# Kernel optimization log

Measured on AMD Instinct MI355X. Metric: run time of the kernel, lower is better.

## Reference

```python
import jax, jax.numpy as jnp
import numpy as np

SIM_THRESHOLD = 0.7
EPS = 1e-8  # matches torch F.cosine_similarity eps

Q, M, D, C = 4096, 65536, 384, 128


def setup_inputs() -> dict:
    key = jax.random.key(0)
    k1, k2, k3 = jax.random.split(key, 3)
    query_embeddings = jax.random.normal(k1, (Q, D), dtype=jnp.float32)
    memory_embeddings = jax.random.normal(k2, (M, D), dtype=jnp.float32)
    # per-example one-hot-ish label vectors [M, C]
    memory_labels = jax.random.uniform(k3, (M, C), dtype=jnp.float32)
    return {
        "query_embeddings": query_embeddings,
        "memory_embeddings": memory_embeddings,
        "memory_labels": memory_labels,
    }


def _l2_normalize(x):
    n = jnp.sqrt(jnp.sum(x * x, axis=-1, keepdims=True))
    return x / jnp.maximum(n, EPS)


def reference(query_embeddings, memory_embeddings, memory_labels):
    # cosine similarity matrix [Q, M] via normalized GEMM
    qn = _l2_normalize(query_embeddings)          # [Q, D]
    mn = _l2_normalize(memory_embeddings)         # [M, D]
    sims = jnp.einsum("qd,md->qm", qn, mn)        # [Q, M]
    max_sim = jnp.max(sims, axis=1)               # [Q]
    max_idx = jnp.argmax(sims, axis=1)            # [Q]
    picked = memory_labels[max_idx]               # [Q, C] gather
    C_ = memory_labels.shape[1]
    uniform = jnp.full((1, C_), 1.0 / C_, dtype=picked.dtype)
    predictions = jnp.where((max_sim > SIM_THRESHOLD)[:, None], picked, uniform)
    return predictions
```

## Files before the change

### kernel.cpp

```cpp
#include <hip/hip_runtime.h>
#include <math.h>

#define QN 4096
#define MN 65536
#define DN 384
#define CN 128
#define NCHUNK 32
#define MROWS_PER_CHUNK (MN / NCHUNK)
#define MT_PER (MROWS_PER_CHUNK / 128)

typedef __attribute__((ext_vector_type(8))) int i32x8;
typedef __attribute__((ext_vector_type(4))) int i32x4;
typedef __attribute__((ext_vector_type(4))) float f32x4;

__device__ __forceinline__ unsigned char f2fp8(float f) {
  return (unsigned char)(__builtin_amdgcn_cvt_pk_fp8_f32(f, 0.f, 0, false) & 0xff);
}

__device__ __forceinline__ void async16(const void* g, void* l) {
  __builtin_amdgcn_global_load_lds(
      (const __attribute__((address_space(1))) unsigned int*)g,
      (__attribute__((address_space(3))) unsigned int*)l, 16, 0, 0);
}

__global__ __launch_bounds__(256) void nrm_kernel(const float* __restrict__ qe,
                                                  const float* __restrict__ me,
                                                  unsigned char* __restrict__ yq,
                                                  unsigned char* __restrict__ ym) {
  const int row = blockIdx.x * 4 + (threadIdx.x >> 6);
  const int lane = threadIdx.x & 63;
  const float* xr;
  unsigned char* yr;
  if (row < QN) {
    xr = qe + (size_t)row * DN;
    yr = yq + (size_t)row * DN;
  } else {
    xr = me + (size_t)(row - QN) * DN;
    yr = ym + (size_t)(row - QN) * DN;
  }
  float v[6];
  float ss = 0.f;
#pragma unroll
  for (int i = 0; i < 6; ++i) {
    v[i] = xr[lane + i * 64];
    ss += v[i] * v[i];
  }
#pragma unroll
  for (int m = 1; m < 64; m <<= 1) ss += __shfl_xor(ss, m);
  const float scale = 1.0f / fmaxf(sqrtf(ss), 1e-8f);
#pragma unroll
  for (int i = 0; i < 6; ++i) yr[lane + i * 64] = f2fp8(v[i] * scale);
}

__global__ __launch_bounds__(256, 2) void gemm_max_kernel(
    const unsigned char* __restrict__ qn8, const unsigned char* __restrict__ mn8,
    float* __restrict__ pmax) {
  __shared__ unsigned char Bs[128 * DN];
  __shared__ float smax[2][128];

  const int tid = threadIdx.x;
  const int wave = tid >> 6, lane = tid & 63;
  const int wr = wave >> 1, wc = wave & 1;
  const int quad = lane >> 4, l16 = lane & 15;
  const int r7 = l16 & 7;
  const int qrow0 = blockIdx.x * 128;
  const int mchunk0 = blockIdx.y * MROWS_PER_CHUNK;

  int srcoff[12];
#pragma unroll
  for (int i = 0; i < 12; ++i) {
    const int ci = i * 256 + tid;
    const int row = ci / 24;
    const int j = ci - row * 24;
    const int gj = (j & 24) | ((j ^ row) & 7);
    srcoff[i] = row * DN + gj * 16;
  }
  unsigned char* ldsbase[12];
#pragma unroll
  for (int i = 0; i < 12; ++i) ldsbase[i] = &Bs[(i * 256 + wave * 64) * 16];

  float rmax[16];
#pragma unroll
  for (int i = 0; i < 16; ++i) rmax[i] = -3.0e38f;

  {
    const unsigned char* abase = qn8 + (size_t)qrow0 * DN;
#pragma unroll
    for (int i = 0; i < 12; ++i) async16(abase + srcoff[i], ldsbase[i]);
  }
  __syncthreads();
  i32x8 afr[3][4];
#pragma unroll
  for (int kc = 0; kc < 3; ++kc)
#pragma unroll
    for (int rt = 0; rt < 4; ++rt) {
      const unsigned char* p = &Bs[(wr * 64 + rt * 16 + l16) * DN];
      const int clo = kc * 8 + ((quad * 2 + 0) ^ r7);
      const int chi = kc * 8 + ((quad * 2 + 1) ^ r7);
      i32x4 lo = *(const i32x4*)&p[clo * 16];
      i32x4 hi = *(const i32x4*)&p[chi * 16];
      afr[kc][rt][0] = lo[0]; afr[kc][rt][1] = lo[1];
      afr[kc][rt][2] = lo[2]; afr[kc][rt][3] = lo[3];
      afr[kc][rt][4] = hi[0]; afr[kc][rt][5] = hi[1];
      afr[kc][rt][6] = hi[2]; afr[kc][rt][7] = hi[3];
    }
  __syncthreads();

#pragma unroll 1
  for (int mt = 0; mt < MT_PER; ++mt) {
    const unsigned char* bbase = mn8 + (size_t)(mchunk0 + mt * 128) * DN;
#pragma unroll
    for (int i = 0; i < 12; ++i) async16(bbase + srcoff[i], ldsbase[i]);

    f32x4 acc[4][4];
#pragma unroll
    for (int rt = 0; rt < 4; ++rt)
#pragma unroll
      for (int ct = 0; ct < 4; ++ct) acc[rt][ct] = (f32x4){0.f, 0.f, 0.f, 0.f};

    __syncthreads();
#pragma unroll
    for (int kc = 0; kc < 3; ++kc) {
      i32x8 bfr[4];
#pragma unroll
      for (int ct = 0; ct < 4; ++ct) {
        const unsigned char* p = &Bs[(wc * 64 + ct * 16 + l16) * DN];
        const int clo = kc * 8 + ((quad * 2 + 0) ^ r7);
        const int chi = kc * 8 + ((quad * 2 + 1) ^ r7);
        i32x4 lo = *(const i32x4*)&p[clo * 16];
        i32x4 hi = *(const i32x4*)&p[chi * 16];
        bfr[ct][0] = lo[0]; bfr[ct][1] = lo[1];
        bfr[ct][2] = lo[2]; bfr[ct][3] = lo[3];
        bfr[ct][4] = hi[0]; bfr[ct][5] = hi[1];
        bfr[ct][6] = hi[2]; bfr[ct][7] = hi[3];
      }
#pragma unroll
      for (int rt = 0; rt < 4; ++rt)
#pragma unroll
        for (int ct = 0; ct < 4; ++ct)
          acc[rt][ct] = __builtin_amdgcn_mfma_scale_f32_16x16x128_f8f6f4(
              afr[kc][rt], bfr[ct], acc[rt][ct], 0, 0,
              0, 0x7f7f7f7f, 0, 0x7f7f7f7f);
    }
    __syncthreads();

#pragma unroll
    for (int rt = 0; rt < 4; ++rt)
#pragma unroll
      for (int r = 0; r < 4; ++r) {
        float v = fmaxf(fmaxf(acc[rt][0][r], acc[rt][1][r]),
                        fmaxf(acc[rt][2][r], acc[rt][3][r]));
        rmax[rt * 4 + r] = fmaxf(rmax[rt * 4 + r], v);
      }
  }

#pragma unroll
  for (int i = 0; i < 16; ++i) {
    float v = rmax[i];
    v = fmaxf(v, __shfl_xor(v, 1));
    v = fmaxf(v, __shfl_xor(v, 2));
    v = fmaxf(v, __shfl_xor(v, 4));
    v = fmaxf(v, __shfl_xor(v, 8));
    rmax[i] = v;
  }
  if (l16 == 0) {
#pragma unroll
    for (int rt = 0; rt < 4; ++rt)
#pragma unroll
      for (int r = 0; r < 4; ++r)
        smax[wc][wr * 64 + rt * 16 + quad * 4 + r] = rmax[rt * 4 + r];
  }
  __syncthreads();
  if (tid < 128) {
    const float v = fmaxf(smax[0][tid], smax[1][tid]);
    pmax[(size_t)(qrow0 + tid) * NCHUNK + blockIdx.y] = v;
  }
}

__global__ __launch_bounds__(256) void decide_kernel(
    const float* __restrict__ pmax, const float* __restrict__ qe,
    const float* __restrict__ me, const float* __restrict__ labels,
    float* __restrict__ out) {
  const int q = blockIdx.x;
  const int t = threadIdx.x;
  __shared__ float smx;
  if (t < 64) {
    float v = (t < NCHUNK) ? pmax[(size_t)q * NCHUNK + t] : -3.0e38f;
#pragma unroll
    for (int m = 1; m < 64; m <<= 1) v = fmaxf(v, __shfl_xor(v, m));
    if (t == 0) smx = v;
  }
  __syncthreads();
  if (smx <= 0.5f) {
    if (t < CN) out[(size_t)q * CN + t] = 1.0f / 128.0f;
    return;
  }
  __shared__ float sred[256];
  __shared__ int sidx[256];
  __shared__ float wsum[4];
  const float* qr = qe + (size_t)q * DN;
  float ss = 0.f;
  for (int i = t; i < DN; i += 256) ss += qr[i] * qr[i];
#pragma unroll
  for (int m = 1; m < 64; m <<= 1) ss += __shfl_xor(ss, m);
  if ((t & 63) == 0) wsum[t >> 6] = ss;
  __syncthreads();
  const float qnorm = fmaxf(sqrtf(wsum[0] + wsum[1] + wsum[2] + wsum[3]), 1e-8f);

  float best = -3.0e38f;
  int bidx = 0x7fffffff;
  for (int j = t; j < MN; j += 256) {
    const float* mr = me + (size_t)j * DN;
    float dot = 0.f, ms = 0.f;
    for (int k = 0; k < DN; ++k) {
      float a = qr[k], b = mr[k];
      dot += a * b;
      ms += b * b;
    }
    const float sim = dot / (qnorm * fmaxf(sqrtf(ms), 1e-8f));
    if (sim > best) { best = sim; bidx = j; }
  }
  sred[t] = best;
  sidx[t] = bidx;
  __syncthreads();
  for (int s = 128; s > 0; s >>= 1) {
    if (t < s) {
      const float ov = sred[t + s];
      const int oi = sidx[t + s];
      if (ov > sred[t] || (ov == sred[t] && oi < sidx[t])) {
        sred[t] = ov;
        sidx[t] = oi;
      }
    }
    __syncthreads();
  }
  const float mx = sred[0];
  const int mi = sidx[0];
  if (t < CN)
    out[(size_t)q * CN + t] =
        (mx > 0.7f) ? labels[(size_t)mi * CN + t] : (1.0f / 128.0f);
}

extern "C" void kernel_launch(void* const* d_in, const int* in_sizes, int n_in,
                              void* d_out, int out_size, void* d_ws,
                              size_t ws_size, hipStream_t stream) {
  const float* qe = (const float*)d_in[0];
  const float* me = (const float*)d_in[1];
  const float* lb = (const float*)d_in[2];
  float* out = (float*)d_out;

  char* ws = (char*)d_ws;
  const size_t OFF_QN = 0;
  const size_t OFF_MN = OFF_QN + (size_t)QN * DN;
  const size_t OFF_PMAX = OFF_MN + (size_t)MN * DN;
  unsigned char* qn8 = (unsigned char*)(ws + OFF_QN);
  unsigned char* mn8 = (unsigned char*)(ws + OFF_MN);
  float* pmax = (float*)(ws + OFF_PMAX);

  nrm_kernel<<<(QN + MN) / 4, 256, 0, stream>>>(qe, me, qn8, mn8);
  gemm_max_kernel<<<dim3(QN / 128, NCHUNK), 256, 0, stream>>>(qn8, mn8, pmax);
  decide_kernel<<<QN, 256, 0, stream>>>(pmax, qe, me, lb, out);
}
```

Before: 256.7 us.

## Double-buffer B tiles with smaller 64-row tiles and more chunks

Splits each memory chunk into 64-row B tiles held in two LDS buffers so the async global-to-LDS load of the next tile overlaps MFMA work on the current one, removing one barrier per iteration. NCHUNK doubles to 64 and launch bounds ask for three blocks per CU, increasing parallelism. The smaller tile halves the per-wave MFMA count per B load, lowering reuse of the A fragments.

```diff
diff --git a/kernel.cpp b/kernel.cpp
--- a/kernel.cpp
+++ b/kernel.cpp
@@ -5,9 +5,10 @@
 #define MN 65536
 #define DN 384
 #define CN 128
-#define NCHUNK 32
+#define NCHUNK 64
 #define MROWS_PER_CHUNK (MN / NCHUNK)
-#define MT_PER (MROWS_PER_CHUNK / 128)
+#define MT_PER (MROWS_PER_CHUNK / 64)
+#define BTILE_B (64 * DN)
 
 typedef __attribute__((ext_vector_type(8))) int i32x8;
 typedef __attribute__((ext_vector_type(4))) int i32x4;
@@ -52,10 +53,10 @@
   for (int i = 0; i < 6; ++i) yr[lane + i * 64] = f2fp8(v[i] * scale);
 }
 
-__global__ __launch_bounds__(256, 2) void gemm_max_kernel(
+__global__ __launch_bounds__(256, 3) void gemm_max_kernel(
     const unsigned char* __restrict__ qn8, const unsigned char* __restrict__ mn8,
     float* __restrict__ pmax) {
-  __shared__ unsigned char Bs[128 * DN];
+  __shared__ unsigned char Bs[2 * BTILE_B];
   __shared__ float smax[2][128];
 
   const int tid = threadIdx.x;
@@ -66,69 +67,78 @@
   const int qrow0 = blockIdx.x * 128;
   const int mchunk0 = blockIdx.y * MROWS_PER_CHUNK;
 
-  int srcoff[12];
-#pragma unroll
-  for (int i = 0; i < 12; ++i) {
+  float rmax[16];
+#pragma unroll
+  for (int i = 0; i < 16; ++i) rmax[i] = -3.0e38f;
+
+  {
+    const unsigned char* abase = qn8 + (size_t)qrow0 * DN;
+#pragma unroll
+    for (int i = 0; i < 12; ++i) {
+      const int ci = i * 256 + tid;
+      const int row = ci / 24;
+      const int j = ci - row * 24;
+      const int gj = (j & 24) | ((j ^ row) & 7);
+      async16(abase + row * DN + gj * 16, &Bs[(i * 256 + wave * 64) * 16]);
+    }
+  }
+  __syncthreads();
+  i32x8 afr[3][4];
+#pragma unroll
+  for (int kc = 0; kc < 3; ++kc)
+#pragma unroll
+    for (int rt = 0; rt < 4; ++rt) {
+      const unsigned char* p = &Bs[(wr * 64 + rt * 16 + l16) * DN];
+      i32x4 lo = *(const i32x4*)&p[(kc * 8 + ((quad * 2 + 0) ^ r7)) * 16];
+      i32x4 hi = *(const i32x4*)&p[(kc * 8 + ((quad * 2 + 1) ^ r7)) * 16];
+      afr[kc][rt][0] = lo[0]; afr[kc][rt][1] = lo[1];
+      afr[kc][rt][2] = lo[2]; afr[kc][rt][3] = lo[3];
+      afr[kc][rt][4] = hi[0]; afr[kc][rt][5] = hi[1];
+      afr[kc][rt][6] = hi[2]; afr[kc][rt][7] = hi[3];
+    }
+  __syncthreads();
+
+  int srcoff[6];
+#pragma unroll
+  for (int i = 0; i < 6; ++i) {
     const int ci = i * 256 + tid;
     const int row = ci / 24;
     const int j = ci - row * 24;
     const int gj = (j & 24) | ((j ^ row) & 7);
     srcoff[i] = row * DN + gj * 16;
   }
-  unsigned char* ldsbase[12];
-#pragma unroll
-  for (int i = 0; i < 12; ++i) ldsbase[i] = &Bs[(i * 256 + wave * 64) * 16];
-
-  float rmax[16];
-#pragma unroll
-  for (int i = 0; i < 16; ++i) rmax[i] = -3.0e38f;
-
-  {
-    const unsigned char* abase = qn8 + (size_t)qrow0 * DN;
-#pragma unroll
-    for (int i = 0; i < 12; ++i) async16(abase + srcoff[i], ldsbase[i]);
-  }
-  __syncthreads();
-  i32x8 afr[3][4];
-#pragma unroll
-  for (int kc = 0; kc < 3; ++kc)
-#pragma unroll
-    for (int rt = 0; rt < 4; ++rt) {
-      const unsigned char* p = &Bs[(wr * 64 + rt * 16 + l16) * DN];
-      const int clo = kc * 8 + ((quad * 2 + 0) ^ r7);
-      const int chi = kc * 8 + ((quad * 2 + 1) ^ r7);
-      i32x4 lo = *(const i32x4*)&p[clo * 16];
-      i32x4 hi = *(const i32x4*)&p[chi * 16];
-      afr[kc][rt][0] = lo[0]; afr[kc][rt][1] = lo[1];
-      afr[kc][rt][2] = lo[2]; afr[kc][rt][3] = lo[3];
-      afr[kc][rt][4] = hi[0]; afr[kc][rt][5] = hi[1];
-      afr[kc][rt][6] = hi[2]; afr[kc][rt][7] = hi[3];
-    }
-  __syncthreads();
+
+  const unsigned char* bchunk = mn8 + (size_t)mchunk0 * DN;
+#pragma unroll
+  for (int i = 0; i < 6; ++i)
+    async16(bchunk + srcoff[i], &Bs[(i * 256 + wave * 64) * 16]);
 
 #pragma unroll 1
   for (int mt = 0; mt < MT_PER; ++mt) {
-    const unsigned char* bbase = mn8 + (size_t)(mchunk0 + mt * 128) * DN;
-#pragma unroll
-    for (int i = 0; i < 12; ++i) async16(bbase + srcoff[i], ldsbase[i]);
-
-    f32x4 acc[4][4];
+    __syncthreads();
+    unsigned char* cur = &Bs[(mt & 1) * BTILE_B];
+    if (mt + 1 < MT_PER) {
+      unsigned char* nxt = &Bs[((mt + 1) & 1) * BTILE_B];
+      const unsigned char* nb = bchunk + (size_t)(mt + 1) * BTILE_B;
+#pragma unroll
+      for (int i = 0; i < 6; ++i)
+        async16(nb + srcoff[i], &nxt[(i * 256 + wave * 64) * 16]);
+    }
+
+    f32x4 acc[4][2];
 #pragma unroll
     for (int rt = 0; rt < 4; ++rt)
 #pragma unroll
-      for (int ct = 0; ct < 4; ++ct) acc[rt][ct] = (f32x4){0.f, 0.f, 0.f, 0.f};
-
-    __syncthreads();
+      for (int ct = 0; ct < 2; ++ct) acc[rt][ct] = (f32x4){0.f, 0.f, 0.f, 0.f};
+
 #pragma unroll
     for (int kc = 0; kc < 3; ++kc) {
-      i32x8 bfr[4];
-#pragma unroll
-      for (int ct = 0; ct < 4; ++ct) {
-        const unsigned char* p = &Bs[(wc * 64 + ct * 16 + l16) * DN];
-        const int clo = kc * 8 + ((quad * 2 + 0) ^ r7);
-        const int chi = kc * 8 + ((quad * 2 + 1) ^ r7);
-        i32x4 lo = *(const i32x4*)&p[clo * 16];
-        i32x4 hi = *(const i32x4*)&p[chi * 16];
+      i32x8 bfr[2];
+#pragma unroll
+      for (int ct = 0; ct < 2; ++ct) {
+        const unsigned char* p = &cur[(wc * 32 + ct * 16 + l16) * DN];
+        i32x4 lo = *(const i32x4*)&p[(kc * 8 + ((quad * 2 + 0) ^ r7)) * 16];
+        i32x4 hi = *(const i32x4*)&p[(kc * 8 + ((quad * 2 + 1) ^ r7)) * 16];
         bfr[ct][0] = lo[0]; bfr[ct][1] = lo[1];
         bfr[ct][2] = lo[2]; bfr[ct][3] = lo[3];
         bfr[ct][4] = hi[0]; bfr[ct][5] = hi[1];
@@ -137,19 +147,17 @@
 #pragma unroll
       for (int rt = 0; rt < 4; ++rt)
 #pragma unroll
-        for (int ct = 0; ct < 4; ++ct)
+        for (int ct = 0; ct < 2; ++ct)
           acc[rt][ct] = __builtin_amdgcn_mfma_scale_f32_16x16x128_f8f6f4(
               afr[kc][rt], bfr[ct], acc[rt][ct], 0, 0,
               0, 0x7f7f7f7f, 0, 0x7f7f7f7f);
     }
-    __syncthreads();
 
 #pragma unroll
     for (int rt = 0; rt < 4; ++rt)
 #pragma unroll
       for (int r = 0; r < 4; ++r) {
-        float v = fmaxf(fmaxf(acc[rt][0][r], acc[rt][1][r]),
-                        fmaxf(acc[rt][2][r], acc[rt][3][r]));
+        const float v = fmaxf(acc[rt][0][r], acc[rt][1][r]);
         rmax[rt * 4 + r] = fmaxf(rmax[rt * 4 + r], v);
       }
   }
@@ -185,7 +193,7 @@
   const int t = threadIdx.x;
   __shared__ float smx;
   if (t < 64) {
-    float v = (t < NCHUNK) ? pmax[(size_t)q * NCHUNK + t] : -3.0e38f;
+    float v = pmax[(size_t)q * NCHUNK + t];
 #pragma unroll
     for (int m = 1; m < 64; m <<= 1) v = fmaxf(v, __shfl_xor(v, m));
     if (t == 0) smx = v;
```

Measured after the change: 301.4 us. 1.17x slower.
